# Kernel optimization log

Measured on AMD Instinct MI355X. Metric: run time of the kernel, lower is better.

Reference implementation:

```python
import jax, jax.numpy as jnp
import numpy as np
from jax import lax


def _binarize(w):
    # XNOR-style sign binarization: sign(w) with sign(0) -> +1
    return jnp.where(w >= 0, 1.0, -1.0).astype(w.dtype)


def setup_inputs() -> dict:
    key = jax.random.key(0)
    kx, kw = jax.random.split(key)
    X = jax.random.normal(kx, (32, 256, 56, 56), dtype=jnp.float32)   # NCHW
    W = jax.random.normal(kw, (256, 256, 3, 3), dtype=jnp.float32)    # OIHW
    return {"X": X, "W": W}


def reference(X, W):
    Wb = _binarize(W)
    # F.conv2d default: padding=0 (VALID), stride=1
    out = lax.conv_general_dilated(
        X, Wb,
        window_strides=(1, 1),
        padding="VALID",
        dimension_numbers=("NCHW", "OIHW", "NCHW"),
    )
    return out  # [32, 256, 54, 54]
```

## Files before the change

kernel.cpp:

```cpp
#include <hip/hip_runtime.h>
#include <stdint.h>

typedef float f32x4 __attribute__((ext_vector_type(4)));
typedef __bf16 bf16x8 __attribute__((ext_vector_type(8)));
typedef unsigned short u16x8 __attribute__((ext_vector_type(8)));
typedef uint32_t u32x2 __attribute__((ext_vector_type(2)));

#define NIMG 32
#define CIN  256
#define HWIN 3136
#define COUT 256
#define HWOUT 2916
#define NPOS 93312

#define XT_BYTES   ((size_t)NIMG*HWIN*CIN*2)
#define WB_OFF     (XT_BYTES + 8192)
#define WB_BYTES   ((size_t)36*4*64*8)
#define WS_NEED    (WB_OFF + WB_BYTES)

static __device__ __forceinline__ unsigned short f2bf(float f) {
    union { float f; uint32_t u; } v; v.f = f;
    return (unsigned short)((v.u + 0x7FFFu + ((v.u >> 16) & 1u)) >> 16);
}

static __device__ __forceinline__ void gload16(const void* g, void* l) {
    __builtin_amdgcn_global_load_lds(
        (const __attribute__((address_space(1))) void*)g,
        (__attribute__((address_space(3))) void*)l, 16, 0, 0);
}

static __device__ __forceinline__ uint32_t lds_a(const void* p) {
    return (uint32_t)(uintptr_t)(__attribute__((address_space(3))) const void*)p;
}

static __device__ __forceinline__ u16x8 ldsr(uint32_t addr) {
    u16x8 r;
    asm volatile("ds_read_b128 %0, %1" : "=v"(r) : "v"(addr));
    return r;
}

static __device__ __forceinline__ u16x8 expand8(uint32_t b) {
    union { uint32_t d[4]; u16x8 v; } u;
    #pragma unroll
    for (int j = 0; j < 4; ++j) {
        uint32_t lo = ((b << (15 - 2 * j)) & 0x8000u) | 0x3F803F80u;
        u.d[j] = ((b << (30 - 2 * j)) & 0x80000000u) | lo;
    }
    return u.v;
}

#define BAR()   __builtin_amdgcn_s_barrier()
#define SCB()   __builtin_amdgcn_sched_barrier(0)
#define LGKM0() do { asm volatile("s_waitcnt lgkmcnt(0)" ::: "memory"); SCB(); } while (0)
#define VM0()   do { asm volatile("s_waitcnt vmcnt(0)" ::: "memory"); SCB(); } while (0)
#define PRIO1() __builtin_amdgcn_s_setprio(1)
#define PRIO0() __builtin_amdgcn_s_setprio(0)

#define MF(a_, b_, c_) __builtin_amdgcn_mfma_f32_16x16x32_bf16( \
    __builtin_bit_cast(bf16x8, a_), __builtin_bit_cast(bf16x8, b_), c_, 0, 0, 0)

#define CLUSTER(A0_, A1_, A2_, A3_, B0_, B1_, B2_, B3_) do {                       \
    acc[0][0]=MF(A0_,B0_,acc[0][0]); acc[1][0]=MF(A1_,B0_,acc[1][0]);              \
    acc[2][0]=MF(A2_,B0_,acc[2][0]); acc[3][0]=MF(A3_,B0_,acc[3][0]);              \
    acc[0][1]=MF(A0_,B1_,acc[0][1]); acc[1][1]=MF(A1_,B1_,acc[1][1]);              \
    acc[2][1]=MF(A2_,B1_,acc[2][1]); acc[3][1]=MF(A3_,B1_,acc[3][1]);              \
    acc[0][2]=MF(A0_,B2_,acc[0][2]); acc[1][2]=MF(A1_,B2_,acc[1][2]);              \
    acc[2][2]=MF(A2_,B2_,acc[2][2]); acc[3][2]=MF(A3_,B2_,acc[3][2]);              \
    acc[0][3]=MF(A0_,B3_,acc[0][3]); acc[1][3]=MF(A1_,B3_,acc[1][3]);              \
    acc[2][3]=MF(A2_,B3_,acc[2][3]); acc[3][3]=MF(A3_,B3_,acc[3][3]);              \
} while (0)

#define EXPANDA(D0_, D1_, D2_, D3_, BW_, h_) do {                       \
    D0_ = expand8(((BW_)[0] >> ((h_) * 8)) & 0xFFu);                    \
    D1_ = expand8(((BW_)[0] >> (16 + (h_) * 8)) & 0xFFu);               \
    D2_ = expand8(((BW_)[1] >> ((h_) * 8)) & 0xFFu);                    \
    D3_ = expand8(((BW_)[1] >> (16 + (h_) * 8)) & 0xFFu);               \
} while (0)

#define BITSLOAD(DST_, kt_) do {                                        \
    const char* _pb = pWb + (uint32_t)(kt_) * 2048u;                    \
    asm volatile("global_load_dwordx2 %0, %1, off"                      \
                 : "=v"(DST_) : "v"(_pb));                              \
} while (0)

__global__ void wbits_k(const float* __restrict__ W, uint32_t* __restrict__ Wb) {
    int tau = blockIdx.x * 256 + threadIdx.x;
    int lane = tau & 63;
    int wr   = (tau >> 6) & 1;
    int ob   = (tau >> 7) & 1;
    int kt   = tau >> 8;
    int l15 = lane & 15, lg = lane >> 4;
    int k9 = kt >> 2;
    int cbase = (kt & 3) * 64 + lg * 8;
    int obase = ob * 128 + wr * 64 + l15;
    uint32_t d0 = 0, d1 = 0;
    #pragma unroll
    for (int m = 0; m < 4; ++m) {
        #pragma unroll
        for (int h = 0; h < 2; ++h) {
            uint32_t b = 0;
            #pragma unroll
            for (int j = 0; j < 8; ++j) {
                int o = obase + m * 16;
                int c = cbase + h * 32 + j;
                float w = W[((size_t)o * 256 + c) * 9 + k9];
                b |= (w < 0.0f ? 1u : 0u) << j;
            }
            int idx = m * 2 + h;
            if (idx < 4) d0 |= b << (idx * 8);
            else         d1 |= b << ((idx - 4) * 8);
        }
    }
    Wb[(size_t)tau * 2 + 0] = d0;
    Wb[(size_t)tau * 2 + 1] = d1;
}

__global__ void xxform(const float* __restrict__ X, unsigned short* __restrict__ Xt) {
    __shared__ float tile[32][65];
    int bid = blockIdx.x;
    int hwc = bid % 49;
    int cc  = (bid / 49) & 7;
    int n   = bid / (49 * 8);
    int hw0 = hwc * 64;
    int c0  = cc * 32;
    int t = threadIdx.x;
    {
        int c = t >> 3;
        int w = (t & 7) * 8;
        const float* src = X + (size_t)(n * CIN + c0 + c) * HWIN + hw0 + w;
        float4 a = *(const float4*)src;
        float4 b = *(const float4*)(src + 4);
        tile[c][w + 0] = a.x; tile[c][w + 1] = a.y; tile[c][w + 2] = a.z; tile[c][w + 3] = a.w;
        tile[c][w + 4] = b.x; tile[c][w + 5] = b.y; tile[c][w + 6] = b.z; tile[c][w + 7] = b.w;
    }
    __syncthreads();
    {
        int w  = t >> 2;
        int cb = (t & 3) * 8;
        u16x8 v;
        #pragma unroll
        for (int j = 0; j < 8; ++j) v[j] = f2bf(tile[cb + j][w]);
        *(u16x8*)(Xt + (size_t)(n * HWIN + hw0 + w) * 256 + c0 + cb) = v;
    }
}

__global__ __launch_bounds__(256, 2)
void bconv_gemm(const unsigned short* __restrict__ Xt,
                const char* __restrict__ Wb,
                float* __restrict__ out) {
    __shared__ __align__(16) char smem[32768];

    const int t    = threadIdx.x;
    const int wid  = t >> 6;
    const int lane = t & 63;
    const int l15  = lane & 15;
    const int lg   = lane >> 4;
    const int wr   = wid >> 1;
    const int wc   = wid & 1;

    const uint32_t bid = blockIdx.x;
    const uint32_t xcd = bid & 7u;
    const uint32_t j8  = bid >> 3;
    const uint32_t swz = (xcd < 2u ? xcd * 183u : 366u + (xcd - 2u) * 182u) + j8;
    const int      ob  = (int)(swz & 1u);
    const uint32_t P0  = (swz >> 1) * 128u;

    const uint32_t colxB = (uint32_t)(((t & 7) ^ ((t >> 3) & 7)) << 4);
    const uint32_t rowt  = (uint32_t)(t >> 3);

    const char* pWb = Wb + ((size_t)(ob * 2 + wr) * 512) + (size_t)lane * 8;

    const char* bB[4];
    #pragma unroll
    for (int r = 0; r < 4; ++r) {
        uint32_t pos = P0 + (uint32_t)(r * 32) + rowt;
        uint32_t ni = pos / (uint32_t)HWOUT;
        uint32_t rm = pos - ni * HWOUT;
        uint32_t ph = rm / 54u;
        uint32_t pw = rm - ph * 54u;
        bB[r] = (const char*)Xt + (size_t)(ni * HWIN + ph * 56u + pw) * 512 + colxB;
    }

    const uint32_t x7  = (uint32_t)(l15 & 7);
    const uint32_t ck0 = ((((uint32_t)lg) ^ x7) << 4);
    const uint32_t ck1 = (((4u | (uint32_t)lg) ^ x7) << 4);
    const uint32_t br0 = (uint32_t)(wc * 64 + 0 * 16 + l15) * 128u;
    const uint32_t br1 = (uint32_t)(wc * 64 + 1 * 16 + l15) * 128u;
    const uint32_t br2 = (uint32_t)(wc * 64 + 2 * 16 + l15) * 128u;
    const uint32_t br3 = (uint32_t)(wc * 64 + 3 * 16 + l15) * 128u;

    const uint32_t E = lds_a(smem);
    const uint32_t O = E + 16384u;

    f32x4 acc[4][4];
    #pragma unroll
    for (int m = 0; m < 4; ++m)
        #pragma unroll
        for (int n = 0; n < 4; ++n)
            acc[m][n] = (f32x4){0.f, 0.f, 0.f, 0.f};

    auto STAGEB = [&](uint32_t bufoff, uint32_t kof) {
        #pragma unroll
        for (int r = 0; r < 4; ++r)
            gload16(bB[r] + kof, smem + bufoff + r * 4096 + (size_t)t * 16);
    };

    uint32_t cc2 = 2, k32 = 0, koff2 = 256;

    u32x2 bE, bO;
    u16x8 a0, a1, a2, a3;
    u16x8 c0, c1, c2, c3;
    u16x8 U0, U1, U2, U3, V0, V1, V2, V3;

    STAGEB(0u, 0u);
    STAGEB(16384u, 128u);
    BITSLOAD(bE, 0);
    BITSLOAD(bO, 1);
    VM0();
    BAR();
    SCB();
    U0 = ldsr(E + br0 + ck0); U1 = ldsr(E + br1 + ck0);
    U2 = ldsr(E + br2 + ck0); U3 = ldsr(E + br3 + ck0);
    LGKM0();

#define GITER(kt_, CUR, NXT, CUROFF, BC, F_ST, F_CONT) do {                  \
    V0 = ldsr((CUR) + br0 + ck1); V1 = ldsr((CUR) + br1 + ck1);              \
    V2 = ldsr((CUR) + br2 + ck1); V3 = ldsr((CUR) + br3 + ck1);              \
    EXPANDA(a0, a1, a2, a3, BC, 0);                                          \
    SCB();                                                                   \
    PRIO1(); CLUSTER(a0, a1, a2, a3, U0, U1, U2, U3); PRIO0();               \
    LGKM0();                       \
    EXPANDA(c0, c1, c2, c3, BC, 1);                                          \
    VM0();           \
    BAR(); SCB();                                                            \
    if (F_ST) {                                                              \
        STAGEB(CUROFF, koff2);                                               \
        if (cc2 == 3) { cc2 = 0;                                             \
            koff2 += ((k32 == 2) ? 54u : 1u) * 512u - 384u;                  \
            k32 = (k32 == 2) ? 0u : k32 + 1u; }                              \
        else { cc2++; koff2 += 128u; }                                       \
        BITSLOAD(BC, (kt_) + 2);                                             \
    }                                                                        \
    if (F_CONT) {                                                            \
        U0 = ldsr((NXT) + br0 + ck0); U1 = ldsr((NXT) + br1 + ck0);          \
        U2 = ldsr((NXT) + br2 + ck0); U3 = ldsr((NXT) + br3 + ck0);          \
        SCB();                                                               \
    }                                                                        \
    PRIO1(); CLUSTER(c0, c1, c2, c3, V0, V1, V2, V3); PRIO0();               \
    if (F_CONT) { LGKM0(); }                                                 \
} while (0)

    for (int g = 0; g < 17; ++g) {
        GITER(2 * g,     E, O, 0u,      bE, 1, 1);
        GITER(2 * g + 1, O, E, 16384u,  bO, 1, 1);
    }
    GITER(34, E, O, 0u,     bE, 0, 1);
    GITER(35, O, E, 16384u, bO, 0, 0);

#undef GITER

    const int orow0 = ob * 128 + wr * 64;
    #pragma unroll
    for (int n = 0; n < 4; ++n) {
        uint32_t P = P0 + (uint32_t)(wc * 64 + n * 16 + l15);
        uint32_t ni = P / (uint32_t)HWOUT;
        uint32_t rm = P - ni * HWOUT;
        float* ob_ = out + (size_t)(ni * 256u + orow0) * HWOUT + rm;
        #pragma unroll
        for (int m = 0; m < 4; ++m)
            #pragma unroll
            for (int r = 0; r < 4; ++r)
                ob_[(size_t)(m * 16 + lg * 4 + r) * HWOUT] = acc[m][n][r];
    }
}

__global__ void bconv_fallback(const float* __restrict__ X, const float* __restrict__ W,
                               float* __restrict__ out) {
    size_t idx = (size_t)blockIdx.x * 256 + threadIdx.x;
    int ow = (int)(idx % 54);
    int oh = (int)((idx / 54) % 54);
    int o  = (int)((idx / 2916) % 256);
    int n  = (int)(idx / 746496);
    float s = 0.f;
    for (int c = 0; c < 256; ++c) {
        const float* xr = X + ((size_t)(n * 256 + c) * 56 + oh) * 56 + ow;
        const float* wr = W + (size_t)(o * 256 + c) * 9;
        #pragma unroll
        for (int kh = 0; kh < 3; ++kh)
            #pragma unroll
            for (int kw = 0; kw < 3; ++kw) {
                float w = wr[kh * 3 + kw];
                float x = xr[kh * 56 + kw];
                s += (w >= 0.f) ? x : -x;
            }
    }
    out[idx] = s;
}

extern "C" void kernel_launch(void* const* d_in, const int* in_sizes, int n_in,
                              void* d_out, int out_size, void* d_ws, size_t ws_size,
                              hipStream_t stream) {
    const float* X = (const float*)d_in[0];
    const float* W = (const float*)d_in[1];
    float* out = (float*)d_out;

    if (ws_size < WS_NEED) {
        bconv_fallback<<<93312, 256, 0, stream>>>(X, W, out);
        return;
    }
    unsigned short* Xt = (unsigned short*)d_ws;
    uint32_t* Wb = (uint32_t*)((char*)d_ws + WB_OFF);

    wbits_k<<<36, 256, 0, stream>>>(W, Wb);
    xxform<<<12544, 256, 0, stream>>>(X, Xt);

    bconv_gemm<<<1458, 256, 0, stream>>>(Xt, (const char*)Wb, out);
}
```

Before: 155.9 us.

## Store weight signs as pre-shifted byte masks and expand with v_perm

The weight-bit kernel now writes each sign as a byte holding only the 0x80 bit, in a 64-byte-per-lane layout. The main kernel expands these masks into bf16 ±1 values with v_perm plus an OR, replacing the shift-and-mask expand8 sequence and cutting VALU work in the MFMA loop. Weight loads become four dwordx4 loads issued one k-step ahead. Wait points move to partial vmcnt(4) waits so activation staging overlaps the weight prefetch. This raises weight memory traffic and register pressure from the extra prefetch registers.

```diff
diff --git a/kernel.cpp b/kernel.cpp
--- a/kernel.cpp
+++ b/kernel.cpp
@@ -4,7 +4,7 @@
 typedef float f32x4 __attribute__((ext_vector_type(4)));
 typedef __bf16 bf16x8 __attribute__((ext_vector_type(8)));
 typedef unsigned short u16x8 __attribute__((ext_vector_type(8)));
-typedef uint32_t u32x2 __attribute__((ext_vector_type(2)));
+typedef uint32_t u32x4 __attribute__((ext_vector_type(4)));
 
 #define NIMG 32
 #define CIN  256
@@ -15,7 +15,7 @@
 
 #define XT_BYTES   ((size_t)NIMG*HWIN*CIN*2)
 #define WB_OFF     (XT_BYTES + 8192)
-#define WB_BYTES   ((size_t)36*4*64*8)
+#define WB_BYTES   ((size_t)36*4*64*64)
 #define WS_NEED    (WB_OFF + WB_BYTES)
 
 static __device__ __forceinline__ unsigned short f2bf(float f) {
@@ -39,20 +39,11 @@
     return r;
 }
 
-static __device__ __forceinline__ u16x8 expand8(uint32_t b) {
-    union { uint32_t d[4]; u16x8 v; } u;
-    #pragma unroll
-    for (int j = 0; j < 4; ++j) {
-        uint32_t lo = ((b << (15 - 2 * j)) & 0x8000u) | 0x3F803F80u;
-        u.d[j] = ((b << (30 - 2 * j)) & 0x80000000u) | lo;
-    }
-    return u.v;
-}
-
 #define BAR()   __builtin_amdgcn_s_barrier()
 #define SCB()   __builtin_amdgcn_sched_barrier(0)
 #define LGKM0() do { asm volatile("s_waitcnt lgkmcnt(0)" ::: "memory"); SCB(); } while (0)
 #define VM0()   do { asm volatile("s_waitcnt vmcnt(0)" ::: "memory"); SCB(); } while (0)
+#define VMC4()  do { asm volatile("s_waitcnt vmcnt(4)" ::: "memory"); SCB(); } while (0)
 #define PRIO1() __builtin_amdgcn_s_setprio(1)
 #define PRIO0() __builtin_amdgcn_s_setprio(0)
 
@@ -70,49 +61,61 @@
     acc[2][3]=MF(A2_,B3_,acc[2][3]); acc[3][3]=MF(A3_,B3_,acc[3][3]);              \
 } while (0)
 
-#define EXPANDA(D0_, D1_, D2_, D3_, BW_, h_) do {                       \
-    D0_ = expand8(((BW_)[0] >> ((h_) * 8)) & 0xFFu);                    \
-    D1_ = expand8(((BW_)[0] >> (16 + (h_) * 8)) & 0xFFu);               \
-    D2_ = expand8(((BW_)[1] >> ((h_) * 8)) & 0xFFu);                    \
-    D3_ = expand8(((BW_)[1] >> (16 + (h_) * 8)) & 0xFFu);               \
+#define EXPH(D0_, D1_, D2_, D3_, QA_, QB_) do {                                     \
+    union { uint32_t d[4]; u16x8 v; } _e0, _e1, _e2, _e3;                           \
+    _e0.d[0] = 0x3F803F80u | __builtin_amdgcn_perm(QA_[0], QA_[0], 0x010C000Cu);    \
+    _e0.d[1] = 0x3F803F80u | __builtin_amdgcn_perm(QA_[0], QA_[0], 0x030C020Cu);    \
+    _e0.d[2] = 0x3F803F80u | __builtin_amdgcn_perm(QA_[1], QA_[1], 0x010C000Cu);    \
+    _e0.d[3] = 0x3F803F80u | __builtin_amdgcn_perm(QA_[1], QA_[1], 0x030C020Cu);    \
+    _e1.d[0] = 0x3F803F80u | __builtin_amdgcn_perm(QA_[2], QA_[2], 0x010C000Cu);    \
+    _e1.d[1] = 0x3F803F80u | __builtin_amdgcn_perm(QA_[2], QA_[2], 0x030C020Cu);    \
+    _e1.d[2] = 0x3F803F80u | __builtin_amdgcn_perm(QA_[3], QA_[3], 0x010C000Cu);    \
+    _e1.d[3] = 0x3F803F80u | __builtin_amdgcn_perm(QA_[3], QA_[3], 0x030C020Cu);    \
+    _e2.d[0] = 0x3F803F80u | __builtin_amdgcn_perm(QB_[0], QB_[0], 0x010C000Cu);    \
+    _e2.d[1] = 0x3F803F80u | __builtin_amdgcn_perm(QB_[0], QB_[0], 0x030C020Cu);    \
+    _e2.d[2] = 0x3F803F80u | __builtin_amdgcn_perm(QB_[1], QB_[1], 0x010C000Cu);    \
+    _e2.d[3] = 0x3F803F80u | __builtin_amdgcn_perm(QB_[1], QB_[1], 0x030C020Cu);    \
+    _e3.d[0] = 0x3F803F80u | __builtin_amdgcn_perm(QB_[2], QB_[2], 0x010C000Cu);    \
+    _e3.d[1] = 0x3F803F80u | __builtin_amdgcn_perm(QB_[2], QB_[2], 0x030C020Cu);    \
+    _e3.d[2] = 0x3F803F80u | __builtin_amdgcn_perm(QB_[3], QB_[3], 0x010C000Cu);    \
+    _e3.d[3] = 0x3F803F80u | __builtin_amdgcn_perm(QB_[3], QB_[3], 0x030C020Cu);    \
+    D0_ = _e0.v; D1_ = _e1.v; D2_ = _e2.v; D3_ = _e3.v;                             \
 } while (0)
 
-#define BITSLOAD(DST_, kt_) do {                                        \
-    const char* _pb = pWb + (uint32_t)(kt_) * 2048u;                    \
-    asm volatile("global_load_dwordx2 %0, %1, off"                      \
-                 : "=v"(DST_) : "v"(_pb));                              \
+#define SLOAD(QN, kt_) do {                                                         \
+    const char* _p = pWb + (uint32_t)(kt_) * 16384u;                                \
+    asm volatile("global_load_dwordx4 %0, %1, off"           : "=v"(QN##0) : "v"(_p)); \
+    asm volatile("global_load_dwordx4 %0, %1, off offset:16" : "=v"(QN##1) : "v"(_p)); \
+    asm volatile("global_load_dwordx4 %0, %1, off offset:32" : "=v"(QN##2) : "v"(_p)); \
+    asm volatile("global_load_dwordx4 %0, %1, off offset:48" : "=v"(QN##3) : "v"(_p)); \
 } while (0)
 
 __global__ void wbits_k(const float* __restrict__ W, uint32_t* __restrict__ Wb) {
-    int tau = blockIdx.x * 256 + threadIdx.x;
-    int lane = tau & 63;
-    int wr   = (tau >> 6) & 1;
-    int ob   = (tau >> 7) & 1;
-    int kt   = tau >> 8;
+    int kt = blockIdx.x;
+    int t  = threadIdx.x;
+    int lane = t & 63;
+    int wr   = (t >> 6) & 1;
+    int ob   = t >> 7;
     int l15 = lane & 15, lg = lane >> 4;
     int k9 = kt >> 2;
-    int cbase = (kt & 3) * 64 + lg * 8;
+    int cb = (kt & 3) * 64 + lg * 8;
     int obase = ob * 128 + wr * 64 + l15;
-    uint32_t d0 = 0, d1 = 0;
-    #pragma unroll
-    for (int m = 0; m < 4; ++m) {
-        #pragma unroll
-        for (int h = 0; h < 2; ++h) {
-            uint32_t b = 0;
+    uint32_t d[16];
+    #pragma unroll
+    for (int i = 0; i < 16; ++i) d[i] = 0;
+    #pragma unroll
+    for (int h = 0; h < 2; ++h)
+        #pragma unroll
+        for (int m = 0; m < 4; ++m)
             #pragma unroll
             for (int j = 0; j < 8; ++j) {
-                int o = obase + m * 16;
-                int c = cbase + h * 32 + j;
-                float w = W[((size_t)o * 256 + c) * 9 + k9];
-                b |= (w < 0.0f ? 1u : 0u) << j;
+                float w = W[((size_t)(obase + m * 16) * 256 + (cb + h * 32 + j)) * 9 + k9];
+                if (w < 0.0f) d[h * 8 + m * 2 + (j >> 2)] |= 0x80u << ((j & 3) * 8);
             }
-            int idx = m * 2 + h;
-            if (idx < 4) d0 |= b << (idx * 8);
-            else         d1 |= b << ((idx - 4) * 8);
-        }
-    }
-    Wb[(size_t)tau * 2 + 0] = d0;
-    Wb[(size_t)tau * 2 + 1] = d1;
+    uint32_t* dst = Wb + ((size_t)((kt * 4 + ob * 2 + wr) * 64 + lane)) * 16;
+    #pragma unroll
+    for (int q = 0; q < 4; ++q)
+        *(u32x4*)(dst + q * 4) = (u32x4){d[q*4+0], d[q*4+1], d[q*4+2], d[q*4+3]};
 }
 
 __global__ void xxform(const float* __restrict__ X, unsigned short* __restrict__ Xt) {
@@ -168,7 +171,7 @@
     const uint32_t colxB = (uint32_t)(((t & 7) ^ ((t >> 3) & 7)) << 4);
     const uint32_t rowt  = (uint32_t)(t >> 3);
 
-    const char* pWb = Wb + ((size_t)(ob * 2 + wr) * 512) + (size_t)lane * 8;
+    const char* pWb = Wb + ((size_t)((ob * 2 + wr) * 64 + lane)) * 64;
 
     const char* bB[4];
     #pragma unroll
@@ -207,43 +210,44 @@
 
     uint32_t cc2 = 2, k32 = 0, koff2 = 256;
 
-    u32x2 bE, bO;
+    u32x4 SE0, SE1, SE2, SE3, SO0, SO1, SO2, SO3;
     u16x8 a0, a1, a2, a3;
     u16x8 c0, c1, c2, c3;
     u16x8 U0, U1, U2, U3, V0, V1, V2, V3;
 
     STAGEB(0u, 0u);
     STAGEB(16384u, 128u);
-    BITSLOAD(bE, 0);
-    BITSLOAD(bO, 1);
+    SLOAD(SE, 0);
     VM0();
     BAR();
     SCB();
     U0 = ldsr(E + br0 + ck0); U1 = ldsr(E + br1 + ck0);
     U2 = ldsr(E + br2 + ck0); U3 = ldsr(E + br3 + ck0);
     LGKM0();
-
-#define GITER(kt_, CUR, NXT, CUROFF, BC, F_ST, F_CONT) do {                  \
+    EXPH(a0, a1, a2, a3, SE0, SE1);
+
+#define GITER(kt_, CUR, NXT, CUROFF, SC, SN, F_LA, F_ST, F_CONT) do {        \
     V0 = ldsr((CUR) + br0 + ck1); V1 = ldsr((CUR) + br1 + ck1);              \
     V2 = ldsr((CUR) + br2 + ck1); V3 = ldsr((CUR) + br3 + ck1);              \
-    EXPANDA(a0, a1, a2, a3, BC, 0);                                          \
+    if (F_LA) { SLOAD(SN, (kt_) + 1); }                                      \
+    EXPH(c0, c1, c2, c3, SC##2, SC##3);                                      \
     SCB();                                                                   \
     PRIO1(); CLUSTER(a0, a1, a2, a3, U0, U1, U2, U3); PRIO0();               \
     LGKM0();                       \
-    EXPANDA(c0, c1, c2, c3, BC, 1);                                          \
-    VM0();           \
-    BAR(); SCB();                                                            \
-    if (F_ST) {                                                              \
-        STAGEB(CUROFF, koff2);                                               \
-        if (cc2 == 3) { cc2 = 0;                                             \
-            koff2 += ((k32 == 2) ? 54u : 1u) * 512u - 384u;                  \
-            k32 = (k32 == 2) ? 0u : k32 + 1u; }                              \
-        else { cc2++; koff2 += 128u; }                                       \
-        BITSLOAD(BC, (kt_) + 2);                                             \
-    }                                                                        \
     if (F_CONT) {                                                            \
+        VMC4();       \
+        BAR(); SCB();                                                        \
+        if (F_ST) {                                                          \
+            STAGEB(CUROFF, koff2);                                           \
+            if (cc2 == 3) { cc2 = 0;                                         \
+                koff2 += ((k32 == 2) ? 54u : 1u) * 512u - 384u;              \
+                k32 = (k32 == 2) ? 0u : k32 + 1u; }                          \
+            else { cc2++; koff2 += 128u; }                                   \
+        }                                                                    \
         U0 = ldsr((NXT) + br0 + ck0); U1 = ldsr((NXT) + br1 + ck0);          \
         U2 = ldsr((NXT) + br2 + ck0); U3 = ldsr((NXT) + br3 + ck0);          \
+        if (F_ST) { VMC4(); } else { VM0(); }         \
+        EXPH(a0, a1, a2, a3, SN##0, SN##1);                                  \
         SCB();                                                               \
     }                                                                        \
     PRIO1(); CLUSTER(c0, c1, c2, c3, V0, V1, V2, V3); PRIO0();               \
@@ -251,11 +255,11 @@
 } while (0)
 
     for (int g = 0; g < 17; ++g) {
-        GITER(2 * g,     E, O, 0u,      bE, 1, 1);
-        GITER(2 * g + 1, O, E, 16384u,  bO, 1, 1);
-    }
-    GITER(34, E, O, 0u,     bE, 0, 1);
-    GITER(35, O, E, 16384u, bO, 0, 0);
+        GITER(2 * g,     E, O, 0u,      SE, SO, 1, 1, 1);
+        GITER(2 * g + 1, O, E, 16384u,  SO, SE, 1, 1, 1);
+    }
+    GITER(34, E, O, 0u,     SE, SO, 1, 0, 1);
+    GITER(35, O, E, 16384u, SO, SE, 0, 0, 0);
 
 #undef GITER
 
```

New measurement: 143.7 us. 1.08x faster.
